# Optimization experiments

Hardware: AMD Instinct MI355X
Metric: run time of the kernel (lower is better)

Reference implementation:

```python
import jax, jax.numpy as jnp
import numpy as np

N = 50000      # node_num
DIN = 128      # input_dim
DH = 128       # hidden_dim
DE = 128       # embedding_dim
DD = 128       # decoder_dim
NE = 800000    # num edges (before self loops)
B = 4096       # drug pairs
EPS = 1e-5


def setup_inputs() -> dict:
    key = jax.random.key(0)
    ks = jax.random.split(key, 16)
    x = jax.random.normal(ks[0], (N, DIN), jnp.float32)
    edge_index = jax.random.randint(ks[1], (2, NE), 0, N, dtype=jnp.int32)
    drug_index = jax.random.randint(ks[2], (B, 2), 0, N, dtype=jnp.int32)
    s = 0.05  # weight scale for numerical sanity
    return {
        "x": x,
        "edge_index": edge_index,
        "drug_index": drug_index,
        "w1": jax.random.normal(ks[3], (DIN, DH), jnp.float32) * s,
        "b1": jnp.zeros((DH,), jnp.float32),
        "w2": jax.random.normal(ks[4], (DH, DH), jnp.float32) * s,
        "b2": jnp.zeros((DH,), jnp.float32),
        "w3": jax.random.normal(ks[5], (DH, DE), jnp.float32) * s,
        "b3": jnp.zeros((DE,), jnp.float32),
        "g1": jnp.ones((DH,), jnp.float32), "be1": jnp.zeros((DH,), jnp.float32),
        "g2": jnp.ones((DH,), jnp.float32), "be2": jnp.zeros((DH,), jnp.float32),
        "g3": jnp.ones((DE,), jnp.float32), "be3": jnp.zeros((DE,), jnp.float32),
        "p1": jax.random.normal(ks[6], (DE, DD), jnp.float32) * s,
        "p2": jax.random.normal(ks[7], (DD, DD), jnp.float32) * s,
    }


def gcn_conv(x, row, col, W, b):
    # row/col already include self loops; PyG: message from row (source), aggregated at col (target)
    n = x.shape[0]
    h = x @ W + b                                   # linear first, as in GCNConv.forward
    deg = jnp.zeros((n,), h.dtype).at[col].add(1.0)  # degree(col) incl. self loops -> >= 1
    dis = deg ** -0.5
    norm = dis[row] * dis[col]                      # [E+N]
    msg = norm[:, None] * h[row]                    # [E+N, d] gather
    return jax.ops.segment_sum(msg, col, num_segments=n)  # scatter-add


def batch_norm(x, gamma, beta):
    m = jnp.mean(x, axis=0)
    v = jnp.mean((x - m) ** 2, axis=0)  # biased var, as torch BatchNorm training
    return (x - m) * jax.lax.rsqrt(v + EPS) * gamma + beta


def leaky(x):
    return jnp.where(x >= 0, x, 0.1 * x)  # LeakyReLU(0.1)


def reference(x, edge_index, drug_index, w1, b1, w2, b2, w3, b3,
              g1, be1, g2, be2, g3, be3, p1, p2):
    n = x.shape[0]
    self_loop = jnp.arange(n, dtype=edge_index.dtype)
    row = jnp.concatenate([edge_index[0], self_loop])
    col = jnp.concatenate([edge_index[1], self_loop])

    h = leaky(batch_norm(gcn_conv(x, row, col, w1, b1), g1, be1))
    h = leaky(batch_norm(gcn_conv(h, row, col, w2, b2), g2, be2))
    h = leaky(batch_norm(gcn_conv(h, row, col, w3, b3), g3, be3))

    di = drug_index.reshape(-1, 2)
    a = h[di[:, 0] - 1]  # [B, DE] (1-based indices; -1 wraps like torch negative index)
    bb = h[di[:, 1] - 1]  # [B, DE]
    t = a @ p1 @ p2 @ p1.T            # [B, DE] bilinear decode, batched
    ypred = jnp.sum(t * bb, axis=1, keepdims=True)  # [B, 1]
    return ypred
```

## Files before the change

kernel.cpp:

```cpp
#include <hip/hip_runtime.h>

#define PAD 64
#define NSLOT 64

__global__ void init_kernel(int* __restrict__ cnt, int n) {
  int i = blockIdx.x * blockDim.x + threadIdx.x;
  int stride = gridDim.x * blockDim.x;
  for (int j = i; j < n; j += stride) cnt[j] = 0;
}

__global__ void fillcsr_kernel(const int* __restrict__ row, const int* __restrict__ col,
                               int* __restrict__ cnt, int* __restrict__ csr, int ne,
                               float* __restrict__ stats, int nstat) {
  int gid = blockIdx.x * blockDim.x + threadIdx.x;
  int stride = gridDim.x * blockDim.x;
  for (int j = gid; j < nstat; j += stride) stats[j] = 0.f;
  if (gid < ne) {
    int d = col[gid];
    int p = atomicAdd(&cnt[d], 1);
    if (p < PAD) csr[d * PAD + p] = row[gid];
  }
}

__global__ __launch_bounds__(256, 4) void gemm_kernel(
    const float* __restrict__ A, const float* __restrict__ W, const float* __restrict__ bias,
    float* __restrict__ out, int n, float invN,
    const float* __restrict__ bn_sum, const float* __restrict__ bn_sq,
    const float* __restrict__ bn_g, const float* __restrict__ bn_b, int use_bn,
    const int* __restrict__ cnt, int gb,
    const float* __restrict__ P, const float* __restrict__ Q, float* __restrict__ Mo,
    int bilin_mode) {
  __shared__ float Ws[32 * 128];
  __shared__ float xs[32 * 128];
  __shared__ float bnsc[128], bnsh[128];
  int tid = threadIdx.x;

  if ((int)blockIdx.x >= gb) {
    int i = blockIdx.x - gb;
    if (tid < 128) bnsc[tid] = P[i * 128 + tid];
    __syncthreads();
    int j = tid & 127, kh = tid >> 7;
    float acc = 0.f;
    if (bilin_mode == 1) {
      for (int k = kh * 64; k < kh * 64 + 64; ++k) acc = fmaf(bnsc[k], Q[k * 128 + j], acc);
    } else {
      const float* qr = Q + (size_t)j * 128;
      for (int l = kh * 64; l < kh * 64 + 64; ++l) acc = fmaf(bnsc[l], qr[l], acc);
    }
    xs[tid] = acc;
    __syncthreads();
    if (tid < 128) Mo[i * 128 + tid] = xs[tid] + xs[128 + tid];
    return;
  }

  if (tid < 128) {
    if (use_bn) {
      float s = 0.f, q = 0.f;
      for (int r2 = 0; r2 < NSLOT; ++r2) { s += bn_sum[r2 * 128 + tid]; q += bn_sq[r2 * 128 + tid]; }
      float m = s * invN;
      float var = q * invN - m * m;
      float rs = rsqrtf(var + 1e-5f);
      float sc = rs * bn_g[tid];
      bnsc[tid] = sc;
      bnsh[tid] = bn_b[tid] - m * sc;
    } else {
      bnsc[tid] = 1.f; bnsh[tid] = 0.f;
    }
  }
  int base = blockIdx.x * 128;
  int tx = tid & 15, ty = tid >> 4;
  int c0 = tx * 4, r0 = ty * 4;
  int r = tid & 127;
  int row_s = base + r;
  int hf = tid >> 7;
  int kw = tid >> 5;
  int c4 = tid & 31;
  const float4* Arow = (const float4*)(A + (size_t)row_s * 128);
  float acc[8][8];
#pragma unroll
  for (int i = 0; i < 8; ++i)
#pragma unroll
    for (int j = 0; j < 8; ++j) acc[i][j] = 0.f;

  for (int kp = 0; kp < 4; ++kp) {
    __syncthreads();
#pragma unroll
    for (int it = 0; it < 4; ++it) {
      int kl = kw + it * 8;
      float4 wv = ((const float4*)(W + (size_t)(kp * 32 + kl) * 128))[c4];
      *(float4*)&Ws[kl * 128 + c4 * 4] = wv;
    }
#pragma unroll
    for (int it = 0; it < 4; ++it) {
      int kbl = hf + it * 2;
      float4 v = make_float4(0.f, 0.f, 0.f, 0.f);
      if (row_s < n) v = Arow[kp * 8 + kbl];
      if (use_bn) {
        int k0 = kp * 32 + kbl * 4;
        float t;
        t = v.x * bnsc[k0 + 0] + bnsh[k0 + 0]; v.x = t >= 0.f ? t : 0.1f * t;
        t = v.y * bnsc[k0 + 1] + bnsh[k0 + 1]; v.y = t >= 0.f ? t : 0.1f * t;
        t = v.z * bnsc[k0 + 2] + bnsh[k0 + 2]; v.z = t >= 0.f ? t : 0.1f * t;
        t = v.w * bnsc[k0 + 3] + bnsh[k0 + 3]; v.w = t >= 0.f ? t : 0.1f * t;
      }
      int kl = kbl * 4;
      xs[(kl + 0) * 128 + r] = v.x;
      xs[(kl + 1) * 128 + r] = v.y;
      xs[(kl + 2) * 128 + r] = v.z;
      xs[(kl + 3) * 128 + r] = v.w;
    }
    __syncthreads();
#pragma unroll 4
    for (int k = 0; k < 32; ++k) {
      float4 a0 = *(const float4*)&xs[k * 128 + r0];
      float4 a1 = *(const float4*)&xs[k * 128 + 64 + r0];
      float4 w0 = *(const float4*)&Ws[k * 128 + c0];
      float4 w1 = *(const float4*)&Ws[k * 128 + 64 + c0];
      float xr[8], wc[8];
      xr[0] = a0.x; xr[1] = a0.y; xr[2] = a0.z; xr[3] = a0.w;
      xr[4] = a1.x; xr[5] = a1.y; xr[6] = a1.z; xr[7] = a1.w;
      wc[0] = w0.x; wc[1] = w0.y; wc[2] = w0.z; wc[3] = w0.w;
      wc[4] = w1.x; wc[5] = w1.y; wc[6] = w1.z; wc[7] = w1.w;
#pragma unroll
      for (int i = 0; i < 8; ++i)
#pragma unroll
        for (int j = 0; j < 8; ++j)
          acc[i][j] = fmaf(xr[i], wc[j], acc[i][j]);
    }
  }
  float bb0[4], bb1[4];
#pragma unroll
  for (int j = 0; j < 4; ++j) { bb0[j] = bias[c0 + j]; bb1[j] = bias[64 + c0 + j]; }
#pragma unroll
  for (int i = 0; i < 8; ++i) {
    int row = base + (i < 4 ? r0 + i : 64 + r0 + (i - 4));
    if (row < n) {
      float rs = rsqrtf((float)(cnt[row] + 1));
      float4 o0, o1;
      o0.x = (acc[i][0] + bb0[0]) * rs; o0.y = (acc[i][1] + bb0[1]) * rs;
      o0.z = (acc[i][2] + bb0[2]) * rs; o0.w = (acc[i][3] + bb0[3]) * rs;
      o1.x = (acc[i][4] + bb1[0]) * rs; o1.y = (acc[i][5] + bb1[1]) * rs;
      o1.z = (acc[i][6] + bb1[2]) * rs; o1.w = (acc[i][7] + bb1[3]) * rs;
      *(float4*)&out[(size_t)row * 128 + c0] = o0;
      *(float4*)&out[(size_t)row * 128 + 64 + c0] = o1;
    }
  }
}

__global__ __launch_bounds__(256) void agg_kernel(const float* __restrict__ z,
                                                  const int* __restrict__ cnt,
                                                  const int* __restrict__ csr,
                                                  float* __restrict__ out,
                                                  float* __restrict__ Ssum,
                                                  float* __restrict__ Ssq,
                                                  int n, int half) {
  __shared__ float bs[4][128], bq[4][128];
  int tid = threadIdx.x;
  int lane = tid & 63;
  int wv = tid >> 6;
  int w = (blockIdx.x * blockDim.x + tid) >> 6;
  float stx = 0.f, sty = 0.f, qtx = 0.f, qty = 0.f;
  if (w < half) {
    int i0 = w, i1 = w + half;
    bool has1 = (i1 < n);
    const float2* __restrict__ h2 = (const float2*)z;
    unsigned off0 = (unsigned)i0 * 64u + (unsigned)lane;
    unsigned off1 = (unsigned)i1 * 64u + (unsigned)lane;
    float2 self0 = h2[off0];
    float2 self1 = has1 ? h2[off1] : make_float2(0.f, 0.f);
    int c0r = cnt[i0];
    int c1r = has1 ? cnt[i1] : 0;
    float d0 = rsqrtf((float)(c0r + 1));
    float d1 = rsqrtf((float)(c1r + 1));
    int e0 = c0r > PAD ? PAD : c0r;
    int e1 = c1r > PAD ? PAD : c1r;
    const int* __restrict__ lp0 = csr + (size_t)i0 * PAD;
    const int* __restrict__ lp1 = csr + (size_t)i1 * PAD;
    float s0x = self0.x, s0y = self0.y;
    float s1x = self1.x, s1y = self1.y;
    int my0 = (lane < e0) ? lp0[lane] : 0;
    int my1 = (lane < e1) ? lp1[lane] : 0;
    int p0 = 0, p1 = 0;
    while (p0 + 8 <= e0 && p1 + 8 <= e1) {
      float2 v0[8], v1[8];
#pragma unroll
      for (int u = 0; u < 8; ++u) { int s = __shfl(my0, p0 + u, 64); v0[u] = h2[(unsigned)s * 64u + (unsigned)lane]; }
#pragma unroll
      for (int u = 0; u < 8; ++u) { int s = __shfl(my1, p1 + u, 64); v1[u] = h2[(unsigned)s * 64u + (unsigned)lane]; }
#pragma unroll
      for (int u = 0; u < 8; ++u) {
        s0x += v0[u].x; s0y += v0[u].y;
        s1x += v1[u].x; s1y += v1[u].y;
      }
      p0 += 8; p1 += 8;
    }
    for (; p0 + 8 <= e0; p0 += 8) {
      float2 v[8];
#pragma unroll
      for (int u = 0; u < 8; ++u) { int s = __shfl(my0, p0 + u, 64); v[u] = h2[(unsigned)s * 64u + (unsigned)lane]; }
#pragma unroll
      for (int u = 0; u < 8; ++u) { s0x += v[u].x; s0y += v[u].y; }
    }
    for (; p0 + 4 <= e0; p0 += 4) {
      float2 v[4];
#pragma unroll
      for (int u = 0; u < 4; ++u) { int s = __shfl(my0, p0 + u, 64); v[u] = h2[(unsigned)s * 64u + (unsigned)lane]; }
#pragma unroll
      for (int u = 0; u < 4; ++u) { s0x += v[u].x; s0y += v[u].y; }
    }
    for (; p0 < e0; ++p0) {
      int s = __shfl(my0, p0, 64);
      float2 v = h2[(unsigned)s * 64u + (unsigned)lane];
      s0x += v.x; s0y += v.y;
    }
    for (; p1 + 8 <= e1; p1 += 8) {
      float2 v[8];
#pragma unroll
      for (int u = 0; u < 8; ++u) { int s = __shfl(my1, p1 + u, 64); v[u] = h2[(unsigned)s * 64u + (unsigned)lane]; }
#pragma unroll
      for (int u = 0; u < 8; ++u) { s1x += v[u].x; s1y += v[u].y; }
    }
    for (; p1 + 4 <= e1; p1 += 4) {
      float2 v[4];
#pragma unroll
      for (int u = 0; u < 4; ++u) { int s = __shfl(my1, p1 + u, 64); v[u] = h2[(unsigned)s * 64u + (unsigned)lane]; }
#pragma unroll
      for (int u = 0; u < 4; ++u) { s1x += v[u].x; s1y += v[u].y; }
    }
    for (; p1 < e1; ++p1) {
      int s = __shfl(my1, p1, 64);
      float2 v = h2[(unsigned)s * 64u + (unsigned)lane];
      s1x += v.x; s1y += v.y;
    }
    float2 o0; o0.x = d0 * s0x; o0.y = d0 * s0y;
    ((float2*)out)[off0] = o0;
    stx += o0.x; qtx = fmaf(o0.x, o0.x, qtx);
    sty += o0.y; qty = fmaf(o0.y, o0.y, qty);
    if (has1) {
      float2 o1; o1.x = d1 * s1x; o1.y = d1 * s1y;
      ((float2*)out)[off1] = o1;
      stx += o1.x; qtx = fmaf(o1.x, o1.x, qtx);
      sty += o1.y; qty = fmaf(o1.y, o1.y, qty);
    }
  }
  bs[wv][2 * lane] = stx;     bs[wv][2 * lane + 1] = sty;
  bq[wv][2 * lane] = qtx;     bq[wv][2 * lane + 1] = qty;
  __syncthreads();
  if (tid < 128) {
    float s = bs[0][tid] + bs[1][tid] + bs[2][tid] + bs[3][tid];
    float q = bq[0][tid] + bq[1][tid] + bq[2][tid] + bq[3][tid];
    int slot = (blockIdx.x & (NSLOT - 1)) * 128 + tid;
    atomicAdd(&Ssum[slot], s);
    atomicAdd(&Ssq[slot], q);
  }
}

__global__ __launch_bounds__(256) void decoder_kernel(
    const float* __restrict__ h, const int* __restrict__ di, const float* __restrict__ M,
    const float* __restrict__ bn_sum, const float* __restrict__ bn_sq,
    const float* __restrict__ bn_g, const float* __restrict__ bn_b,
    float* __restrict__ out, int npairs, int n, float invN) {
  __shared__ float Ms[128 * 128];
  __shared__ float sc[128], sh[128];
  int tid = threadIdx.x;
  if (tid < 128) {
    float s = 0.f, q = 0.f;
    for (int r2 = 0; r2 < NSLOT; ++r2) { s += bn_sum[r2 * 128 + tid]; q += bn_sq[r2 * 128 + tid]; }
    float m = s * invN;
    float var = q * invN - m * m;
    float rs = rsqrtf(var + 1e-5f);
    float scv = rs * bn_g[tid];
    sc[tid] = scv;
    sh[tid] = bn_b[tid] - m * scv;
  }
  for (int t = tid; t < 4096; t += 256) ((float4*)Ms)[t] = ((const float4*)M)[t];
  __syncthreads();
  int lane = tid & 63, wv = tid >> 6;
  int wid = blockIdx.x * 4 + wv;
  int nw = gridDim.x * 4;
  for (int k = wid; k < npairs; k += nw) {
    int ia = di[2 * k] - 1;     if (ia < 0) ia += n;
    int ib = di[2 * k + 1] - 1; if (ib < 0) ib += n;
    const float2* ap2 = (const float2*)(h + (size_t)ia * 128);
    const float* bp = h + (size_t)ib * 128;
    float2 a2 = ap2[lane];
    float ax = a2.x * sc[2 * lane] + sh[2 * lane];         ax = ax >= 0.f ? ax : 0.1f * ax;
    float ay = a2.y * sc[2 * lane + 1] + sh[2 * lane + 1]; ay = ay >= 0.f ? ay : 0.1f * ay;
    float u0 = 0.f, u1 = 0.f;
#pragma unroll 8
    for (int i2 = 0; i2 < 64; ++i2) {
      float avx = __shfl(ax, i2, 64);
      float avy = __shfl(ay, i2, 64);
      int i = 2 * i2;
      u0 = fmaf(avx, Ms[i * 128 + lane], u0);
      u1 = fmaf(avx, Ms[i * 128 + 64 + lane], u1);
      u0 = fmaf(avy, Ms[(i + 1) * 128 + lane], u0);
      u1 = fmaf(avy, Ms[(i + 1) * 128 + 64 + lane], u1);
    }
    float b0 = bp[lane] * sc[lane] + sh[lane];                b0 = b0 >= 0.f ? b0 : 0.1f * b0;
    float b1 = bp[lane + 64] * sc[lane + 64] + sh[lane + 64]; b1 = b1 >= 0.f ? b1 : 0.1f * b1;
    float part = u0 * b0 + u1 * b1;
#pragma unroll
    for (int o = 32; o; o >>= 1) part += __shfl_down(part, o, 64);
    if (lane == 0) out[k] = part;
  }
}

extern "C" void kernel_launch(void* const* d_in, const int* in_sizes, int n_in,
                              void* d_out, int out_size, void* d_ws, size_t ws_size,
                              hipStream_t stream) {
  const float* x   = (const float*)d_in[0];
  const int*   ei  = (const int*)d_in[1];
  const int*   dri = (const int*)d_in[2];
  const float* w1  = (const float*)d_in[3];
  const float* b1  = (const float*)d_in[4];
  const float* w2  = (const float*)d_in[5];
  const float* b2  = (const float*)d_in[6];
  const float* w3  = (const float*)d_in[7];
  const float* b3  = (const float*)d_in[8];
  const float* g1  = (const float*)d_in[9];
  const float* be1 = (const float*)d_in[10];
  const float* g2  = (const float*)d_in[11];
  const float* be2 = (const float*)d_in[12];
  const float* g3  = (const float*)d_in[13];
  const float* be3 = (const float*)d_in[14];
  const float* p1  = (const float*)d_in[15];
  const float* p2  = (const float*)d_in[16];
  float* out = (float*)d_out;

  int n  = in_sizes[0] / 128;
  int ne = in_sizes[1] / 2;
  int np = in_sizes[2] / 2;
  const int* erow = ei;
  const int* ecol = ei + ne;

  size_t o = 0;
  char* wsb = (char*)d_ws;
  auto alloc = [&](size_t bytes) { void* p = wsb + o; o += (bytes + 255) & ~255ull; return p; };
  float* T1   = (float*)alloc((size_t)n * 128 * 4);
  float* T2   = (float*)alloc((size_t)n * 128 * 4);
  int*   csr  = (int*)alloc((size_t)n * PAD * 4);
  int*   cnt  = (int*)alloc((size_t)n * 4);
  int nstat = 6 * NSLOT * 128;
  float* stats = (float*)alloc((size_t)nstat * 4);
  float* Mtmp = (float*)alloc(128 * 128 * 4);
  float* M2   = (float*)alloc(128 * 128 * 4);
  float* Ssum1 = stats;
  float* Ssq1  = stats + 1 * NSLOT * 128;
  float* Ssum2 = stats + 2 * NSLOT * 128;
  float* Ssq2  = stats + 3 * NSLOT * 128;
  float* Ssum3 = stats + 4 * NSLOT * 128;
  float* Ssq3  = stats + 5 * NSLOT * 128;

  float invN = 1.0f / (float)n;
  int eb = (ne + 255) / 256;
  int gb = (n + 127) / 128;
  int half = (n + 1) / 2;
  int ab = (half + 3) / 4;

  init_kernel<<<256, 256, 0, stream>>>(cnt, n);
  fillcsr_kernel<<<eb, 256, 0, stream>>>(erow, ecol, cnt, csr, ne, stats, nstat);

  gemm_kernel<<<gb + 128, 256, 0, stream>>>(x, w1, b1, T1, n, invN,
                                            nullptr, nullptr, nullptr, nullptr, 0, cnt,
                                            gb, p1, p2, Mtmp, 1);
  agg_kernel<<<ab, 256, 0, stream>>>(T1, cnt, csr, T2, Ssum1, Ssq1, n, half);

  gemm_kernel<<<gb + 128, 256, 0, stream>>>(T2, w2, b2, T1, n, invN,
                                            Ssum1, Ssq1, g1, be1, 1, cnt,
                                            gb, Mtmp, p1, M2, 2);
  agg_kernel<<<ab, 256, 0, stream>>>(T1, cnt, csr, T2, Ssum2, Ssq2, n, half);

  gemm_kernel<<<gb, 256, 0, stream>>>(T2, w3, b3, T1, n, invN,
                                      Ssum2, Ssq2, g2, be2, 1, cnt,
                                      gb, nullptr, nullptr, nullptr, 0);
  agg_kernel<<<ab, 256, 0, stream>>>(T1, cnt, csr, T2, Ssum3, Ssq3, n, half);

  decoder_kernel<<<256, 256, 0, stream>>>(T2, dri, M2, Ssum3, Ssq3, g3, be3, out, np, n, invN);
}
```

Measured before the change: 361.9 us.

## Store node features in 16-column slabs and aggregate per slab

Intermediate feature matrices move from row-major [N,128] to eight column slabs of [N,16]. The GEMM writes and reads this blocked layout, and the decoder indexes it. The aggregation kernel is restructured so each block handles a single 16-feature slab for a range of nodes, with a 16-lane group per node. The goal is a smaller per-slab working set (about 3.2MB) that stays cache-resident during random neighbor gathers, at the cost of eight passes over the CSR lists and 64-byte gather granularity instead of 512-byte rows.

```diff
diff --git a/kernel.cpp b/kernel.cpp
--- a/kernel.cpp
+++ b/kernel.cpp
@@ -2,6 +2,7 @@
 
 #define PAD 64
 #define NSLOT 64
+
 
 __global__ void init_kernel(int* __restrict__ cnt, int n) {
   int i = blockIdx.x * blockDim.x + threadIdx.x;
@@ -27,7 +28,7 @@
     float* __restrict__ out, int n, float invN,
     const float* __restrict__ bn_sum, const float* __restrict__ bn_sq,
     const float* __restrict__ bn_g, const float* __restrict__ bn_b, int use_bn,
-    const int* __restrict__ cnt, int gb,
+    const int* __restrict__ cnt, int gb, int in_blocked,
     const float* __restrict__ P, const float* __restrict__ Q, float* __restrict__ Mo,
     int bilin_mode) {
   __shared__ float Ws[32 * 128];
@@ -75,7 +76,6 @@
   int hf = tid >> 7;
   int kw = tid >> 5;
   int c4 = tid & 31;
-  const float4* Arow = (const float4*)(A + (size_t)row_s * 128);
   float acc[8][8];
 #pragma unroll
   for (int i = 0; i < 8; ++i)
@@ -93,15 +93,18 @@
 #pragma unroll
     for (int it = 0; it < 4; ++it) {
       int kbl = hf + it * 2;
+      int c = (kp * 8 + kbl) * 4;
       float4 v = make_float4(0.f, 0.f, 0.f, 0.f);
-      if (row_s < n) v = Arow[kp * 8 + kbl];
+      if (row_s < n) {
+        if (in_blocked) v = *(const float4*)(A + ((size_t)(c >> 4) * n + row_s) * 16 + (c & 15));
+        else            v = *(const float4*)(A + (size_t)row_s * 128 + c);
+      }
       if (use_bn) {
-        int k0 = kp * 32 + kbl * 4;
         float t;
-        t = v.x * bnsc[k0 + 0] + bnsh[k0 + 0]; v.x = t >= 0.f ? t : 0.1f * t;
-        t = v.y * bnsc[k0 + 1] + bnsh[k0 + 1]; v.y = t >= 0.f ? t : 0.1f * t;
-        t = v.z * bnsc[k0 + 2] + bnsh[k0 + 2]; v.z = t >= 0.f ? t : 0.1f * t;
-        t = v.w * bnsc[k0 + 3] + bnsh[k0 + 3]; v.w = t >= 0.f ? t : 0.1f * t;
+        t = v.x * bnsc[c + 0] + bnsh[c + 0]; v.x = t >= 0.f ? t : 0.1f * t;
+        t = v.y * bnsc[c + 1] + bnsh[c + 1]; v.y = t >= 0.f ? t : 0.1f * t;
+        t = v.z * bnsc[c + 2] + bnsh[c + 2]; v.z = t >= 0.f ? t : 0.1f * t;
+        t = v.w * bnsc[c + 3] + bnsh[c + 3]; v.w = t >= 0.f ? t : 0.1f * t;
       }
       int kl = kbl * 4;
       xs[(kl + 0) * 128 + r] = v.x;
@@ -131,6 +134,7 @@
   float bb0[4], bb1[4];
 #pragma unroll
   for (int j = 0; j < 4; ++j) { bb0[j] = bias[c0 + j]; bb1[j] = bias[64 + c0 + j]; }
+  int c1 = 64 + c0;
 #pragma unroll
   for (int i = 0; i < 8; ++i) {
     int row = base + (i < 4 ? r0 + i : 64 + r0 + (i - 4));
@@ -141,8 +145,8 @@
       o0.z = (acc[i][2] + bb0[2]) * rs; o0.w = (acc[i][3] + bb0[3]) * rs;
       o1.x = (acc[i][4] + bb1[0]) * rs; o1.y = (acc[i][5] + bb1[1]) * rs;
       o1.z = (acc[i][6] + bb1[2]) * rs; o1.w = (acc[i][7] + bb1[3]) * rs;
-      *(float4*)&out[(size_t)row * 128 + c0] = o0;
-      *(float4*)&out[(size_t)row * 128 + 64 + c0] = o1;
+      *(float4*)(out + ((size_t)(c0 >> 4) * n + row) * 16 + (c0 & 15)) = o0;
+      *(float4*)(out + ((size_t)(c1 >> 4) * n + row) * 16 + (c1 & 15)) = o1;
     }
   }
 }
@@ -153,105 +157,58 @@
                                                   float* __restrict__ out,
                                                   float* __restrict__ Ssum,
                                                   float* __restrict__ Ssq,
-                                                  int n, int half) {
-  __shared__ float bs[4][128], bq[4][128];
+                                                  int n, int npb) {
+  __shared__ float bs[16], bq[16];
   int tid = threadIdx.x;
-  int lane = tid & 63;
-  int wv = tid >> 6;
-  int w = (blockIdx.x * blockDim.x + tid) >> 6;
-  float stx = 0.f, sty = 0.f, qtx = 0.f, qty = 0.f;
-  if (w < half) {
-    int i0 = w, i1 = w + half;
-    bool has1 = (i1 < n);
-    const float2* __restrict__ h2 = (const float2*)z;
-    unsigned off0 = (unsigned)i0 * 64u + (unsigned)lane;
-    unsigned off1 = (unsigned)i1 * 64u + (unsigned)lane;
-    float2 self0 = h2[off0];
-    float2 self1 = has1 ? h2[off1] : make_float2(0.f, 0.f);
-    int c0r = cnt[i0];
-    int c1r = has1 ? cnt[i1] : 0;
-    float d0 = rsqrtf((float)(c0r + 1));
-    float d1 = rsqrtf((float)(c1r + 1));
-    int e0 = c0r > PAD ? PAD : c0r;
-    int e1 = c1r > PAD ? PAD : c1r;
-    const int* __restrict__ lp0 = csr + (size_t)i0 * PAD;
-    const int* __restrict__ lp1 = csr + (size_t)i1 * PAD;
-    float s0x = self0.x, s0y = self0.y;
-    float s1x = self1.x, s1y = self1.y;
-    int my0 = (lane < e0) ? lp0[lane] : 0;
-    int my1 = (lane < e1) ? lp1[lane] : 0;
-    int p0 = 0, p1 = 0;
-    while (p0 + 8 <= e0 && p1 + 8 <= e1) {
-      float2 v0[8], v1[8];
-#pragma unroll
-      for (int u = 0; u < 8; ++u) { int s = __shfl(my0, p0 + u, 64); v0[u] = h2[(unsigned)s * 64u + (unsigned)lane]; }
-#pragma unroll
-      for (int u = 0; u < 8; ++u) { int s = __shfl(my1, p1 + u, 64); v1[u] = h2[(unsigned)s * 64u + (unsigned)lane]; }
-#pragma unroll
-      for (int u = 0; u < 8; ++u) {
-        s0x += v0[u].x; s0y += v0[u].y;
-        s1x += v1[u].x; s1y += v1[u].y;
+  if (tid < 16) { bs[tid] = 0.f; bq[tid] = 0.f; }
+  __syncthreads();
+  int s = blockIdx.x & 7;
+  int grp = blockIdx.x >> 3;
+  int w = tid >> 6, lane = tid & 63;
+  int g = lane >> 4, t = lane & 15;
+  const float* __restrict__ zs = z + (size_t)s * n * 16;
+  float* __restrict__ os = out + (size_t)s * n * 16;
+  float ps = 0.f, pq = 0.f;
+  int nstart = grp * npb;
+  int nend = nstart + npb; if (nend > n) nend = n;
+  int srcbase = lane & 48;
+  for (int node = nstart + w * 4 + g; node < nend; node += 16) {
+    int rawc = cnt[node];
+    float di = rsqrtf((float)(rawc + 1));
+    int deg = rawc > PAD ? PAD : rawc;
+    const int* __restrict__ lp = csr + (size_t)node * PAD;
+    float acc = zs[(size_t)node * 16 + t];
+    for (int b = 0; b < deg; b += 16) {
+      int rem = deg - b; if (rem > 16) rem = 16;
+      int myidx = (t < rem) ? lp[b + t] : 0;
+      int e = 0;
+      for (; e + 4 <= rem; e += 4) {
+        int s0 = __shfl(myidx, srcbase + e + 0, 64);
+        int s1 = __shfl(myidx, srcbase + e + 1, 64);
+        int s2 = __shfl(myidx, srcbase + e + 2, 64);
+        int s3 = __shfl(myidx, srcbase + e + 3, 64);
+        float v0 = zs[(size_t)s0 * 16 + t];
+        float v1 = zs[(size_t)s1 * 16 + t];
+        float v2 = zs[(size_t)s2 * 16 + t];
+        float v3 = zs[(size_t)s3 * 16 + t];
+        acc += (v0 + v1) + (v2 + v3);
       }
-      p0 += 8; p1 += 8;
-    }
-    for (; p0 + 8 <= e0; p0 += 8) {
-      float2 v[8];
-#pragma unroll
-      for (int u = 0; u < 8; ++u) { int s = __shfl(my0, p0 + u, 64); v[u] = h2[(unsigned)s * 64u + (unsigned)lane]; }
-#pragma unroll
-      for (int u = 0; u < 8; ++u) { s0x += v[u].x; s0y += v[u].y; }
-    }
-    for (; p0 + 4 <= e0; p0 += 4) {
-      float2 v[4];
-#pragma unroll
-      for (int u = 0; u < 4; ++u) { int s = __shfl(my0, p0 + u, 64); v[u] = h2[(unsigned)s * 64u + (unsigned)lane]; }
-#pragma unroll
-      for (int u = 0; u < 4; ++u) { s0x += v[u].x; s0y += v[u].y; }
-    }
-    for (; p0 < e0; ++p0) {
-      int s = __shfl(my0, p0, 64);
-      float2 v = h2[(unsigned)s * 64u + (unsigned)lane];
-      s0x += v.x; s0y += v.y;
-    }
-    for (; p1 + 8 <= e1; p1 += 8) {
-      float2 v[8];
-#pragma unroll
-      for (int u = 0; u < 8; ++u) { int s = __shfl(my1, p1 + u, 64); v[u] = h2[(unsigned)s * 64u + (unsigned)lane]; }
-#pragma unroll
-      for (int u = 0; u < 8; ++u) { s1x += v[u].x; s1y += v[u].y; }
-    }
-    for (; p1 + 4 <= e1; p1 += 4) {
-      float2 v[4];
-#pragma unroll
-      for (int u = 0; u < 4; ++u) { int s = __shfl(my1, p1 + u, 64); v[u] = h2[(unsigned)s * 64u + (unsigned)lane]; }
-#pragma unroll
-      for (int u = 0; u < 4; ++u) { s1x += v[u].x; s1y += v[u].y; }
-    }
-    for (; p1 < e1; ++p1) {
-      int s = __shfl(my1, p1, 64);
-      float2 v = h2[(unsigned)s * 64u + (unsigned)lane];
-      s1x += v.x; s1y += v.y;
-    }
-    float2 o0; o0.x = d0 * s0x; o0.y = d0 * s0y;
-    ((float2*)out)[off0] = o0;
-    stx += o0.x; qtx = fmaf(o0.x, o0.x, qtx);
-    sty += o0.y; qty = fmaf(o0.y, o0.y, qty);
-    if (has1) {
-      float2 o1; o1.x = d1 * s1x; o1.y = d1 * s1y;
-      ((float2*)out)[off1] = o1;
-      stx += o1.x; qtx = fmaf(o1.x, o1.x, qtx);
-      sty += o1.y; qty = fmaf(o1.y, o1.y, qty);
-    }
-  }
-  bs[wv][2 * lane] = stx;     bs[wv][2 * lane + 1] = sty;
-  bq[wv][2 * lane] = qtx;     bq[wv][2 * lane + 1] = qty;
+      for (; e < rem; ++e) {
+        int ss = __shfl(myidx, srcbase + e, 64);
+        acc += zs[(size_t)ss * 16 + t];
+      }
+    }
+    float o = di * acc;
+    os[(size_t)node * 16 + t] = o;
+    ps += o; pq = fmaf(o, o, pq);
+  }
+  atomicAdd(&bs[t], ps);
+  atomicAdd(&bq[t], pq);
   __syncthreads();
-  if (tid < 128) {
-    float s = bs[0][tid] + bs[1][tid] + bs[2][tid] + bs[3][tid];
-    float q = bq[0][tid] + bq[1][tid] + bq[2][tid] + bq[3][tid];
-    int slot = (blockIdx.x & (NSLOT - 1)) * 128 + tid;
-    atomicAdd(&Ssum[slot], s);
-    atomicAdd(&Ssq[slot], q);
+  if (tid < 16) {
+    int slot = (grp & (NSLOT - 1)) * 128 + s * 16 + tid;
+    atomicAdd(&Ssum[slot], bs[tid]);
+    atomicAdd(&Ssq[slot], bq[tid]);
   }
 }
 
@@ -278,14 +235,16 @@
   int lane = tid & 63, wv = tid >> 6;
   int wid = blockIdx.x * 4 + wv;
   int nw = gridDim.x * 4;
+  int f0 = 2 * lane;
+  size_t aoff = ((size_t)(f0 >> 4) * n) * 16 + (f0 & 15);
+  size_t b0off = ((size_t)(lane >> 4) * n) * 16 + (lane & 15);
+  size_t b1off = ((size_t)((lane + 64) >> 4) * n) * 16 + (lane & 15);
   for (int k = wid; k < npairs; k += nw) {
     int ia = di[2 * k] - 1;     if (ia < 0) ia += n;
     int ib = di[2 * k + 1] - 1; if (ib < 0) ib += n;
-    const float2* ap2 = (const float2*)(h + (size_t)ia * 128);
-    const float* bp = h + (size_t)ib * 128;
-    float2 a2 = ap2[lane];
-    float ax = a2.x * sc[2 * lane] + sh[2 * lane];         ax = ax >= 0.f ? ax : 0.1f * ax;
-    float ay = a2.y * sc[2 * lane + 1] + sh[2 * lane + 1]; ay = ay >= 0.f ? ay : 0.1f * ay;
+    float2 a2 = *(const float2*)(h + aoff + (size_t)ia * 16);
+    float ax = a2.x * sc[f0] + sh[f0];         ax = ax >= 0.f ? ax : 0.1f * ax;
+    float ay = a2.y * sc[f0 + 1] + sh[f0 + 1]; ay = ay >= 0.f ? ay : 0.1f * ay;
     float u0 = 0.f, u1 = 0.f;
 #pragma unroll 8
     for (int i2 = 0; i2 < 64; ++i2) {
@@ -297,8 +256,10 @@
       u0 = fmaf(avy, Ms[(i + 1) * 128 + lane], u0);
       u1 = fmaf(avy, Ms[(i + 1) * 128 + 64 + lane], u1);
     }
-    float b0 = bp[lane] * sc[lane] + sh[lane];                b0 = b0 >= 0.f ? b0 : 0.1f * b0;
-    float b1 = bp[lane + 64] * sc[lane + 64] + sh[lane + 64]; b1 = b1 >= 0.f ? b1 : 0.1f * b1;
+    float bv0 = h[b0off + (size_t)ib * 16];
+    float bv1 = h[b1off + (size_t)ib * 16];
+    float b0 = bv0 * sc[lane] + sh[lane];                b0 = b0 >= 0.f ? b0 : 0.1f * b0;
+    float b1 = bv1 * sc[lane + 64] + sh[lane + 64];      b1 = b1 >= 0.f ? b1 : 0.1f * b1;
     float part = u0 * b0 + u1 * b1;
 #pragma unroll
     for (int o = 32; o; o >>= 1) part += __shfl_down(part, o, 64);
@@ -355,26 +316,27 @@
   float invN = 1.0f / (float)n;
   int eb = (ne + 255) / 256;
   int gb = (n + 127) / 128;
-  int half = (n + 1) / 2;
-  int ab = (half + 3) / 4;
+  int grps = 448;
+  int npb = (n + grps - 1) / grps;
+  int ab = grps * 8;
 
   init_kernel<<<256, 256, 0, stream>>>(cnt, n);
   fillcsr_kernel<<<eb, 256, 0, stream>>>(erow, ecol, cnt, csr, ne, stats, nstat);
 
   gemm_kernel<<<gb + 128, 256, 0, stream>>>(x, w1, b1, T1, n, invN,
                                             nullptr, nullptr, nullptr, nullptr, 0, cnt,
-                                            gb, p1, p2, Mtmp, 1);
-  agg_kernel<<<ab, 256, 0, stream>>>(T1, cnt, csr, T2, Ssum1, Ssq1, n, half);
+                                            gb, 0, p1, p2, Mtmp, 1);
+  agg_kernel<<<ab, 256, 0, stream>>>(T1, cnt, csr, T2, Ssum1, Ssq1, n, npb);
 
   gemm_kernel<<<gb + 128, 256, 0, stream>>>(T2, w2, b2, T1, n, invN,
                                             Ssum1, Ssq1, g1, be1, 1, cnt,
-                                            gb, Mtmp, p1, M2, 2);
-  agg_kernel<<<ab, 256, 0, stream>>>(T1, cnt, csr, T2, Ssum2, Ssq2, n, half);
+                                            gb, 1, Mtmp, p1, M2, 2);
+  agg_kernel<<<ab, 256, 0, stream>>>(T1, cnt, csr, T2, Ssum2, Ssq2, n, npb);
 
   gemm_kernel<<<gb, 256, 0, stream>>>(T2, w3, b3, T1, n, invN,
                                       Ssum2, Ssq2, g2, be2, 1, cnt,
-                                      gb, nullptr, nullptr, nullptr, 0);
-  agg_kernel<<<ab, 256, 0, stream>>>(T1, cnt, csr, T2, Ssum3, Ssq3, n, half);
+                                      gb, 1, nullptr, nullptr, nullptr, 0);
+  agg_kernel<<<ab, 256, 0, stream>>>(T1, cnt, csr, T2, Ssum3, Ssq3, n, npb);
 
   decoder_kernel<<<256, 256, 0, stream>>>(T2, dri, M2, Ssum3, Ssq3, g3, be3, out, np, n, invN);
 }
```

Result: slower. 397.0 us (+9.7%).
